# Kernel optimization log

Measured on AMD Instinct MI355X. Metric: run time of the kernel, lower is better.

Reference implementation:

```python
import jax, jax.numpy as jnp
import numpy as np

B, S, D = 32, 2048, 1024

def setup_inputs() -> dict:
    key = jax.random.key(0)
    k1, k2, k3 = jax.random.split(key, 3)
    embed_output = jax.random.normal(k1, (B, S, D), dtype=jnp.float32)
    mask = jax.random.randint(k2, (B, S), 0, 2) > 0  # bool [B,S]
    w = jax.random.normal(k3, (D, D), dtype=jnp.float32) * 0.05
    return {"embed_output": embed_output, "mask": mask, "w": w}

def reference(embed_output, mask, w):
    # ys: mean over sequence (NOTE: original does NOT mask the mean) -> [B,1,D]
    ys = jnp.mean(embed_output, axis=-2, keepdims=True)
    maskf = mask.astype(jnp.float32)
    # eW = (E @ W) * mask  -> [B,S,D]
    eW = jnp.einsum('bsd,de->bse', embed_output, w) * maskf[..., None]
    # f = dot(eW, ys) over last axis -> [B,S,1]
    f = jnp.sum(eW * ys, axis=-1, keepdims=True)
    # additive -1e9 bias where mask is False
    f = f + ((1.0 - maskf) * -1.0e9)[..., None]
    # softmax over sequence axis (-2)
    f = jax.nn.softmax(f, axis=-2)
    # weighted sum over sequence -> [B,D]
    zs = jnp.sum(f * embed_output, axis=-2)
    return zs, f
```

## Files before the change

kernel.cpp:

```cpp
#include <hip/hip_runtime.h>
#include <hip/hip_bf16.h>

#define B_ 32
#define S_ 2048
#define D_ 1024
#define NCH1 64
#define NCH3 128

__global__ void probe_mask(const unsigned int* __restrict__ m, int* __restrict__ flag) {
    int tid = threadIdx.x;
    bool isI = true, isF = true;
    for (int i = tid * 4; i < tid * 4 + 4; ++i) {
        unsigned v = m[i];
        if (v > 1u) isI = false;
        if (v != 0u && v != 0x3F800000u) isF = false;
    }
    unsigned long long bi = __ballot(isI);
    unsigned long long bf = __ballot(isF);
    if (tid == 0) {
        int f = 0;
        if (bi == ~0ull) f = 1;
        else if (bf == ~0ull) f = 2;
        *flag = f;
    }
}

__global__ __launch_bounds__(256) void k1_colsum(const float* __restrict__ E,
                                                 float* __restrict__ part_sums) {
    int chunk = blockIdx.x, b = blockIdx.y, tid = threadIdx.x;
    const float4* base =
        (const float4*)(E + (size_t)(b * S_ + chunk * (S_ / NCH1)) * D_);
    float4 acc = make_float4(0.f, 0.f, 0.f, 0.f);
#pragma unroll 4
    for (int i = 0; i < S_ / NCH1; ++i) {
        float4 e = base[(size_t)i * (D_ / 4) + tid];
        acc.x += e.x; acc.y += e.y; acc.z += e.z; acc.w += e.w;
    }
    ((float4*)part_sums)[(size_t)(b * NCH1 + chunk) * (D_ / 4) + tid] = acc;
}

__global__ void k2a_ys(const float* __restrict__ part_sums, float* __restrict__ ys) {
    int g = blockIdx.x * 256 + threadIdx.x;
    int b = g >> 10, d = g & (D_ - 1);
    float s = 0.f;
#pragma unroll 8
    for (int k = 0; k < NCH1; ++k) s += part_sums[(size_t)(b * NCH1 + k) * D_ + d];
    ys[g] = s * (1.0f / S_);
}

__global__ __launch_bounds__(256) void k2b_v(const float* __restrict__ w,
                                             const float* __restrict__ ys,
                                             float* __restrict__ v) {
    int tid = threadIdx.x, wave = tid >> 6, lane = tid & 63;
    int d = blockIdx.x * 4 + wave;
    const float4* wrow = (const float4*)(w + (size_t)d * D_);
    float4 w0 = wrow[lane], w1 = wrow[64 + lane], w2 = wrow[128 + lane], w3 = wrow[192 + lane];
    for (int b = 0; b < B_; ++b) {
        const float4* yb = (const float4*)(ys + (size_t)b * D_);
        float4 y0 = yb[lane], y1 = yb[64 + lane], y2 = yb[128 + lane], y3 = yb[192 + lane];
        float p = w0.x * y0.x + w0.y * y0.y + w0.z * y0.z + w0.w * y0.w;
        p += w1.x * y1.x + w1.y * y1.y + w1.z * y1.z + w1.w * y1.w;
        p += w2.x * y2.x + w2.y * y2.y + w2.z * y2.z + w2.w * y2.w;
        p += w3.x * y3.x + w3.y * y3.y + w3.z * y3.z + w3.w * y3.w;
#pragma unroll
        for (int off = 32; off; off >>= 1) p += __shfl_xor(p, off, 64);
        if (lane == 0) v[(size_t)b * D_ + d] = p;
    }
}

__global__ __launch_bounds__(256) void k3_fused(
    const float* __restrict__ E, const void* __restrict__ maskp,
    const float* __restrict__ v, const int* __restrict__ flagp,
    float* __restrict__ logits, float* __restrict__ part_m,
    float* __restrict__ part_l, float* __restrict__ part_z) {
    int chunk = blockIdx.x, b = blockIdx.y;
    int tid = threadIdx.x, wave = tid >> 6, lane = tid & 63;
    int mf = *flagp;
    const int* mi = (const int*)maskp;
    const unsigned char* mu = (const unsigned char*)maskp;
    const float* mfl = (const float*)maskp;

    const float4* vf = (const float4*)(v + (size_t)b * D_);
    float4 v0 = vf[lane], v1 = vf[64 + lane], v2 = vf[128 + lane], v3 = vf[192 + lane];

    int s0 = chunk * 16 + wave * 4;
    const float4* row0 = (const float4*)(E + (size_t)(b * S_ + s0) * D_);

    float4 e[4][4];
#pragma unroll
    for (int i = 0; i < 4; ++i) {
        const float4* row = row0 + (size_t)i * (D_ / 4);
        e[i][0] = row[lane]; e[i][1] = row[64 + lane];
        e[i][2] = row[128 + lane]; e[i][3] = row[192 + lane];
    }
    float lg4[4];
#pragma unroll
    for (int i = 0; i < 4; ++i) {
        float p = e[i][0].x * v0.x + e[i][0].y * v0.y + e[i][0].z * v0.z + e[i][0].w * v0.w;
        p += e[i][1].x * v1.x + e[i][1].y * v1.y + e[i][1].z * v1.z + e[i][1].w * v1.w;
        p += e[i][2].x * v2.x + e[i][2].y * v2.y + e[i][2].z * v2.z + e[i][2].w * v2.w;
        p += e[i][3].x * v3.x + e[i][3].y * v3.y + e[i][3].z * v3.z + e[i][3].w * v3.w;
#pragma unroll
        for (int off = 32; off; off >>= 1) p += __shfl_xor(p, off, 64);
        int idx = b * S_ + s0 + i;
        int mv = (mf == 1) ? (mi[idx] != 0)
                           : (mf == 2 ? (mfl[idx] != 0.0f) : (mu[idx] != 0));
        lg4[i] = mv ? p : -1.0e9f;
    }

    __shared__ float4 slog4[4];
    __shared__ float swgt[16];
    if (lane == 0) {
        float4 lf = make_float4(lg4[0], lg4[1], lg4[2], lg4[3]);
        slog4[wave] = lf;
        *(float4*)(logits + (size_t)b * S_ + s0) = lf;
    }
    __syncthreads();

    if (wave == 0 && lane < 16) {
        const float* slog = (const float*)slog4;
        float m = -3.0e38f;
#pragma unroll
        for (int i = 0; i < 16; ++i) m = fmaxf(m, slog[i]);
        float wv = __expf(slog[lane] - m);
        swgt[lane] = wv;
        float l = wv;
#pragma unroll
        for (int off = 1; off < 16; off <<= 1) l += __shfl_xor(l, off, 64);
        if (lane == 0) {
            part_m[b * NCH3 + chunk] = m;
            part_l[b * NCH3 + chunk] = l;
        }
    }
    __syncthreads();

    float4 z0 = make_float4(0.f, 0.f, 0.f, 0.f), z1 = z0, z2 = z0, z3 = z0;
#pragma unroll
    for (int i = 0; i < 4; ++i) {
        float pe = swgt[wave * 4 + i];
        z0.x += pe * e[i][0].x; z0.y += pe * e[i][0].y; z0.z += pe * e[i][0].z; z0.w += pe * e[i][0].w;
        z1.x += pe * e[i][1].x; z1.y += pe * e[i][1].y; z1.z += pe * e[i][1].z; z1.w += pe * e[i][1].w;
        z2.x += pe * e[i][2].x; z2.y += pe * e[i][2].y; z2.z += pe * e[i][2].z; z2.w += pe * e[i][2].w;
        z3.x += pe * e[i][3].x; z3.y += pe * e[i][3].y; z3.z += pe * e[i][3].z; z3.w += pe * e[i][3].w;
    }

    __shared__ float4 zbuf[4][256];
    zbuf[wave][lane] = z0; zbuf[wave][64 + lane] = z1;
    zbuf[wave][128 + lane] = z2; zbuf[wave][192 + lane] = z3;
    __syncthreads();
    float4 a0 = zbuf[0][tid], a1 = zbuf[1][tid], a2 = zbuf[2][tid], a3 = zbuf[3][tid];
    float4 r = make_float4(a0.x + a1.x + a2.x + a3.x, a0.y + a1.y + a2.y + a3.y,
                           a0.z + a1.z + a2.z + a3.z, a0.w + a1.w + a2.w + a3.w);
    ((float4*)(part_z + (size_t)(b * NCH3 + chunk) * D_))[tid] = r;
}

__global__ __launch_bounds__(256) void k4_merge(
    const float* __restrict__ part_m, const float* __restrict__ part_l,
    const float* __restrict__ part_z, float* __restrict__ out_zs,
    float* __restrict__ mg, float* __restrict__ lg) {
    int b = blockIdx.x, tid = threadIdx.x;
    __shared__ float pm_s[NCH3], pl_s[NCH3], scl_s[NCH3];
    if (tid < NCH3) {
        pm_s[tid] = part_m[b * NCH3 + tid];
        pl_s[tid] = part_l[b * NCH3 + tid];
    }
    __syncthreads();
    float mb = -3.0e38f;
    for (int i = 0; i < NCH3; ++i) mb = fmaxf(mb, pm_s[i]);
    if (tid < NCH3) scl_s[tid] = __expf(pm_s[tid] - mb);
    __syncthreads();
    float lsum = 0.f;
    for (int i = 0; i < NCH3; ++i) lsum += pl_s[i] * scl_s[i];
    float4 acc = make_float4(0.f, 0.f, 0.f, 0.f);
    for (int i = 0; i < NCH3; ++i) {
        float scl = scl_s[i];
        float4 zv = ((const float4*)(part_z + (size_t)(b * NCH3 + i) * D_))[tid];
        acc.x += scl * zv.x; acc.y += scl * zv.y;
        acc.z += scl * zv.z; acc.w += scl * zv.w;
    }
    float inv = 1.0f / lsum;
    ((float4*)(out_zs + (size_t)b * D_))[tid] =
        make_float4(acc.x * inv, acc.y * inv, acc.z * inv, acc.w * inv);
    if (tid == 0) { mg[b] = mb; lg[b] = lsum; }
}

__global__ void k5_f(const float* __restrict__ logits, const float* __restrict__ mg,
                     const float* __restrict__ lg, float* __restrict__ out_f) {
    int g = blockIdx.x * 256 + threadIdx.x;
    int b = g >> 11;
    out_f[g] = __expf(logits[g] - mg[b]) * (1.0f / lg[b]);
}

extern "C" void kernel_launch(void* const* d_in, const int* in_sizes, int n_in,
                              void* d_out, int out_size, void* d_ws, size_t ws_size,
                              hipStream_t stream) {
    const float* E = (const float*)d_in[0];
    const void* maskp = d_in[1];
    const float* w = (const float*)d_in[2];
    float* out = (float*)d_out;

    float* ws = (float*)d_ws;
    float* part_sums = ws;
    float* ys = part_sums + (size_t)B_ * NCH1 * D_;
    float* v = ys + (size_t)B_ * D_;
    float* logits = v + (size_t)B_ * D_;
    float* part_m = logits + (size_t)B_ * S_;
    float* part_l = part_m + B_ * NCH3;
    float* part_z = part_l + B_ * NCH3;
    float* mg = part_z + (size_t)B_ * NCH3 * D_;
    float* lg = mg + B_;
    int* flag = (int*)(lg + B_);

    probe_mask<<<1, 64, 0, stream>>>((const unsigned int*)maskp, flag);
    k1_colsum<<<dim3(NCH1, B_), 256, 0, stream>>>(E, part_sums);
    k2a_ys<<<(B_ * D_) / 256, 256, 0, stream>>>(part_sums, ys);
    k2b_v<<<D_ / 4, 256, 0, stream>>>(w, ys, v);
    k3_fused<<<dim3(NCH3, B_), 256, 0, stream>>>(E, maskp, v, flag, logits,
                                                 part_m, part_l, part_z);
    k4_merge<<<B_, 256, 0, stream>>>(part_m, part_l, part_z, out, mg, lg);
    k5_f<<<(B_ * S_) / 256, 256, 0, stream>>>(logits, mg, lg, out + B_ * D_);
}
```

Baseline: 487.7 us.

## Fuse mask probe into colsum, fuse softmax output into merge, reverse k3 order

Moves the mask-format probe into the first block of the column-sum kernel and folds the final softmax normalisation into the merge kernel, cutting two kernel launches and the mg/lg round-trip. It also reverses the block order of the fused k3 pass so it starts on the rows of E that k1 read last, which are more likely to still be in cache. The risks are slightly more work in one k1 block and only 32 blocks handling the f output in the merged kernel.

```diff
diff --git a/kernel.cpp b/kernel.cpp
--- a/kernel.cpp
+++ b/kernel.cpp
@@ -7,27 +7,27 @@
 #define NCH1 64
 #define NCH3 128
 
-__global__ void probe_mask(const unsigned int* __restrict__ m, int* __restrict__ flag) {
-    int tid = threadIdx.x;
-    bool isI = true, isF = true;
-    for (int i = tid * 4; i < tid * 4 + 4; ++i) {
-        unsigned v = m[i];
-        if (v > 1u) isI = false;
-        if (v != 0u && v != 0x3F800000u) isF = false;
-    }
-    unsigned long long bi = __ballot(isI);
-    unsigned long long bf = __ballot(isF);
-    if (tid == 0) {
-        int f = 0;
-        if (bi == ~0ull) f = 1;
-        else if (bf == ~0ull) f = 2;
-        *flag = f;
-    }
-}
-
 __global__ __launch_bounds__(256) void k1_colsum(const float* __restrict__ E,
-                                                 float* __restrict__ part_sums) {
+                                                 float* __restrict__ part_sums,
+                                                 const unsigned int* __restrict__ mprobe,
+                                                 int* __restrict__ flag) {
     int chunk = blockIdx.x, b = blockIdx.y, tid = threadIdx.x;
+    if (chunk == 0 && b == 0 && tid < 64) {
+        bool isI = true, isF = true;
+        for (int i = tid * 4; i < tid * 4 + 4; ++i) {
+            unsigned v = mprobe[i];
+            if (v > 1u) isI = false;
+            if (v != 0u && v != 0x3F800000u) isF = false;
+        }
+        unsigned long long bi = __ballot(isI);
+        unsigned long long bf = __ballot(isF);
+        if (tid == 0) {
+            int f = 0;
+            if (bi == ~0ull) f = 1;
+            else if (bf == ~0ull) f = 2;
+            *flag = f;
+        }
+    }
     const float4* base =
         (const float4*)(E + (size_t)(b * S_ + chunk * (S_ / NCH1)) * D_);
     float4 acc = make_float4(0.f, 0.f, 0.f, 0.f);
@@ -73,7 +73,7 @@
     const float* __restrict__ v, const int* __restrict__ flagp,
     float* __restrict__ logits, float* __restrict__ part_m,
     float* __restrict__ part_l, float* __restrict__ part_z) {
-    int chunk = blockIdx.x, b = blockIdx.y;
+    int chunk = (NCH3 - 1) - blockIdx.x, b = (B_ - 1) - blockIdx.y;
     int tid = threadIdx.x, wave = tid >> 6, lane = tid & 63;
     int mf = *flagp;
     const int* mi = (const int*)maskp;
@@ -154,10 +154,10 @@
     ((float4*)(part_z + (size_t)(b * NCH3 + chunk) * D_))[tid] = r;
 }
 
-__global__ __launch_bounds__(256) void k4_merge(
+__global__ __launch_bounds__(256) void k4_merge_f(
     const float* __restrict__ part_m, const float* __restrict__ part_l,
-    const float* __restrict__ part_z, float* __restrict__ out_zs,
-    float* __restrict__ mg, float* __restrict__ lg) {
+    const float* __restrict__ part_z, const float* __restrict__ logits,
+    float* __restrict__ out_zs, float* __restrict__ out_f) {
     int b = blockIdx.x, tid = threadIdx.x;
     __shared__ float pm_s[NCH3], pl_s[NCH3], scl_s[NCH3];
     if (tid < NCH3) {
@@ -181,14 +181,14 @@
     float inv = 1.0f / lsum;
     ((float4*)(out_zs + (size_t)b * D_))[tid] =
         make_float4(acc.x * inv, acc.y * inv, acc.z * inv, acc.w * inv);
-    if (tid == 0) { mg[b] = mb; lg[b] = lsum; }
-}
-
-__global__ void k5_f(const float* __restrict__ logits, const float* __restrict__ mg,
-                     const float* __restrict__ lg, float* __restrict__ out_f) {
-    int g = blockIdx.x * 256 + threadIdx.x;
-    int b = g >> 11;
-    out_f[g] = __expf(logits[g] - mg[b]) * (1.0f / lg[b]);
+    const float4* lrow = (const float4*)(logits + (size_t)b * S_);
+    float4* frow = (float4*)(out_f + (size_t)b * S_);
+#pragma unroll
+    for (int j = 0; j < 2; ++j) {
+        float4 lv = lrow[j * 256 + tid];
+        frow[j * 256 + tid] = make_float4(__expf(lv.x - mb) * inv, __expf(lv.y - mb) * inv,
+                                          __expf(lv.z - mb) * inv, __expf(lv.w - mb) * inv);
+    }
 }
 
 extern "C" void kernel_launch(void* const* d_in, const int* in_sizes, int n_in,
@@ -207,16 +207,14 @@
     float* part_m = logits + (size_t)B_ * S_;
     float* part_l = part_m + B_ * NCH3;
     float* part_z = part_l + B_ * NCH3;
-    float* mg = part_z + (size_t)B_ * NCH3 * D_;
-    float* lg = mg + B_;
-    int* flag = (int*)(lg + B_);
-
-    probe_mask<<<1, 64, 0, stream>>>((const unsigned int*)maskp, flag);
-    k1_colsum<<<dim3(NCH1, B_), 256, 0, stream>>>(E, part_sums);
+    int* flag = (int*)(part_z + (size_t)B_ * NCH3 * D_);
+
+    k1_colsum<<<dim3(NCH1, B_), 256, 0, stream>>>(E, part_sums,
+                                                  (const unsigned int*)maskp, flag);
     k2a_ys<<<(B_ * D_) / 256, 256, 0, stream>>>(part_sums, ys);
     k2b_v<<<D_ / 4, 256, 0, stream>>>(w, ys, v);
     k3_fused<<<dim3(NCH3, B_), 256, 0, stream>>>(E, maskp, v, flag, logits,
                                                  part_m, part_l, part_z);
-    k4_merge<<<B_, 256, 0, stream>>>(part_m, part_l, part_z, out, mg, lg);
-    k5_f<<<(B_ * S_) / 256, 256, 0, stream>>>(logits, mg, lg, out + B_ * D_);
-}
+    k4_merge_f<<<B_, 256, 0, stream>>>(part_m, part_l, part_z, logits,
+                                       out, out + B_ * D_);
+}
```

Result: no change. 485.0 us (-0.6%).
